# Kernel tuning notes

Hardware: AMD Instinct MI355X
Metric: run time of the kernel (lower is better)

The kernel has to match this reference:

```python
import jax, jax.numpy as jnp
import numpy as np

B, NMASK, DIM, HEADS = 8, 1024, 768, 12
HEAD_DIM = DIM // HEADS
SCALE = HEAD_DIM ** -0.5
NEG = -1e9  # finite stand-in for -inf to keep fully-masked rows NaN-free


def setup_inputs() -> dict:
    key = jax.random.key(0)
    ks = jax.random.split(key, 7)
    x = jax.random.normal(ks[0], (B, NMASK + 1, DIM), dtype=jnp.float32)
    # valid-prefix padding mask (realistic variable-length batch), lengths >= 1
    lengths = jax.random.randint(ks[1], (B,), 1, NMASK + 1)
    mask = jnp.arange(NMASK)[None, :] < lengths[:, None]  # (B, NMASK) bool
    w_qkv = jax.random.normal(ks[2], (DIM, 3 * DIM), dtype=jnp.float32) * (DIM ** -0.5)
    b_qkv = jax.random.normal(ks[3], (3 * DIM,), dtype=jnp.float32) * 0.02
    w_proj = jax.random.normal(ks[4], (DIM, DIM), dtype=jnp.float32) * (DIM ** -0.5)
    b_proj = jax.random.normal(ks[5], (DIM,), dtype=jnp.float32) * 0.02
    return {"x": x, "mask": mask, "w_qkv": w_qkv, "b_qkv": b_qkv,
            "w_proj": w_proj, "b_proj": b_proj}


def reference(x, mask, w_qkv, b_qkv, w_proj, b_proj):
    b, n, _ = x.shape
    qkv = x @ w_qkv + b_qkv                        # (b, n, 3*dim)
    qkv = qkv.reshape(b, n, 3, HEADS, HEAD_DIM)    # 'b n (qkv h d)'
    qkv = jnp.transpose(qkv, (2, 0, 3, 1, 4))      # (3, b, h, n, d)
    q, k, v = qkv[0], qkv[1], qkv[2]
    logits = jnp.einsum('bhid,bhjd->bhij', q, k) * SCALE
    m = jnp.pad(mask, ((0, 0), (1, 0)), constant_values=True)   # prepend CLS=True
    am = m[:, None, :] & m[:, :, None]             # (b, n, n)
    logits = jnp.where(am[:, None, :, :], logits, NEG)
    attn = jax.nn.softmax(logits, axis=-1)
    out = jnp.einsum('bhij,bhjd->bhid', attn, v)   # (b, h, n, d)
    out = jnp.transpose(out, (0, 2, 1, 3)).reshape(b, n, DIM)
    return out @ w_proj + b_proj                   # dropout is identity (eval/p=0)
```

## Files before the change

### kernel.cpp

```cpp
#include <hip/hip_runtime.h>
#include <stdint.h>

#define BATCH   8
#define NMASK_  1024
#define SEQ     1025
#define NPAD    1056
#define DIM     768
#define HEADS   12
#define HD      64
#define BHN     (BATCH*HEADS)
#define MROWS   (BATCH*SEQ)
#define K3      (3*DIM)

typedef unsigned short u16;
typedef __attribute__((ext_vector_type(8))) short s8v;
typedef __attribute__((ext_vector_type(4))) float f4v;
typedef __attribute__((ext_vector_type(4))) unsigned short u16x4;

__device__ __forceinline__ u16 rne_bf16(float f) {
  unsigned u = __float_as_uint(f);
  u += 0x7fffu + ((u >> 16) & 1u);
  return (u16)(u >> 16);
}
__device__ __forceinline__ float bf2f(u16 u) {
  return __uint_as_float(((unsigned)u) << 16);
}

__device__ __forceinline__ void gld16(const u16* g, u16* l) {
  __builtin_amdgcn_global_load_lds(
      (const __attribute__((address_space(1))) void*)g,
      (__attribute__((address_space(3))) void*)l, 16, 0, 0);
}

__device__ __forceinline__ void barrier_() {
  asm volatile("" ::: "memory");
  __builtin_amdgcn_s_barrier();
  asm volatile("" ::: "memory");
}

__global__ __launch_bounds__(256) void k_len(const int* __restrict__ mask,
                                             int* __restrict__ lens) {
  int b = blockIdx.x, t = threadIdx.x;
  int s = 0;
  for (int j = t; j < NMASK_; j += 256) s += (mask[b * NMASK_ + j] != 0) ? 1 : 0;
  __shared__ int red[256];
  red[t] = s; __syncthreads();
  for (int st = 128; st > 0; st >>= 1) { if (t < st) red[t] += red[t + st]; __syncthreads(); }
  if (t == 0) lens[b] = red[0] + 1;
}

__global__ __launch_bounds__(256) void k_cvt_x(const float* __restrict__ x,
                                               u16* __restrict__ xb, int n4) {
  int i = blockIdx.x * 256 + threadIdx.x;
  if (i >= n4) return;
  float4 v = ((const float4*)x)[i];
  u16x4 o;
  o[0] = rne_bf16(v.x); o[1] = rne_bf16(v.y); o[2] = rne_bf16(v.z); o[3] = rne_bf16(v.w);
  *(u16x4*)&xb[i * 4] = o;
}

__global__ __launch_bounds__(256) void k_wT(const float* __restrict__ w,
                                            u16* __restrict__ wT, int R, int C) {
  __shared__ float tile[32][33];
  int c0 = blockIdx.x * 32, r0 = blockIdx.y * 32;
  int tx = threadIdx.x & 31, ty = threadIdx.x >> 5;
  #pragma unroll
  for (int i = 0; i < 32; i += 8) tile[ty + i][tx] = w[(size_t)(r0 + ty + i) * C + c0 + tx];
  __syncthreads();
  #pragma unroll
  for (int i = 0; i < 32; i += 8)
    wT[(size_t)(c0 + ty + i) * R + r0 + tx] = rne_bf16(tile[tx][ty + i]);
}

__global__ __launch_bounds__(256) void k_zpad(u16* __restrict__ VT) {
  int idx = blockIdx.x * 256 + threadIdx.x;
  const int PADW = NPAD - SEQ;
  if (idx >= BHN * HD * PADW) return;
  int c = idx % PADW, rd = idx / PADW;
  VT[(size_t)rd * NPAD + SEQ + c] = 0;
}

__device__ __forceinline__ void gemm_ml128(const u16* __restrict__ A,
                                           const u16* __restrict__ Bt,
                                           int M, int m0, int n0,
                                           f4v acc[4][4], u16* smem) {
  const int t = threadIdx.x;
  const int w = t >> 6, l = t & 63, lg = l >> 4, lr = l & 15;
  const int wr = w >> 1, wc = w & 1;

  int rA0 = m0 + (t >> 2);       if (rA0 >= M) rA0 = M - 1;
  int rA1 = m0 + (t >> 2) + 64;  if (rA1 >= M) rA1 = M - 1;
  const u16* sA0 = A  + (size_t)rA0 * DIM + (t & 3) * 8;
  const u16* sA1 = A  + (size_t)rA1 * DIM + (t & 3) * 8;
  const u16* sB0 = Bt + (size_t)(n0 + (t >> 2)) * DIM + (t & 3) * 8;
  const u16* sB1 = Bt + (size_t)(n0 + (t >> 2) + 64) * DIM + (t & 3) * 8;
  const int dO0 = w * 512, dO1 = 2048 + w * 512;

  #pragma unroll
  for (int fm = 0; fm < 4; fm++)
    #pragma unroll
    for (int fn = 0; fn < 4; fn++) { f4v z = {0.f, 0.f, 0.f, 0.f}; acc[fm][fn] = z; }

  gld16(sA0, &smem[dO0]);        gld16(sA1, &smem[dO1]);
  gld16(sB0, &smem[8192 + dO0]); gld16(sB1, &smem[8192 + dO1]);

  const int NT = DIM / 32;
  for (int kt = 0; kt < NT; ++kt) {
    const int p = kt & 1;
    if (kt + 1 < NT) {
      const int ka = (kt + 1) * 32;
      const int nb = (p ^ 1) * 4096;
      gld16(sA0 + ka, &smem[nb + dO0]);        gld16(sA1 + ka, &smem[nb + dO1]);
      gld16(sB0 + ka, &smem[8192 + nb + dO0]); gld16(sB1 + ka, &smem[8192 + nb + dO1]);
      asm volatile("s_waitcnt vmcnt(4)" ::: "memory");
    } else {
      asm volatile("s_waitcnt vmcnt(0)" ::: "memory");
    }
    __builtin_amdgcn_sched_barrier(0);
    barrier_();
    const u16* lA = &smem[p * 4096];
    const u16* lB = &smem[8192 + p * 4096];
    s8v a[4], bb[4];
    #pragma unroll
    for (int fm = 0; fm < 4; fm++) a[fm] = *(const s8v*)&lA[(wr * 64 + fm * 16 + lr) * 32 + lg * 8];
    #pragma unroll
    for (int fn = 0; fn < 4; fn++) bb[fn] = *(const s8v*)&lB[(wc * 64 + fn * 16 + lr) * 32 + lg * 8];
    #pragma unroll
    for (int fm = 0; fm < 4; fm++)
      #pragma unroll
      for (int fn = 0; fn < 4; fn++)
        acc[fm][fn] = __builtin_amdgcn_mfma_f32_16x16x32_bf16(a[fm], bb[fn], acc[fm][fn], 0, 0, 0);
    barrier_();
  }
}

__global__ __launch_bounds__(256) void k_gemm_qkv(const u16* __restrict__ xb,
                                                  const u16* __restrict__ wqkvT,
                                                  const float* __restrict__ bqkv,
                                                  const int* __restrict__ lens,
                                                  u16* __restrict__ Q,
                                                  u16* __restrict__ Kb,
                                                  u16* __restrict__ VT) {
  __shared__ alignas(16) u16 smem[16384];
  int m0 = blockIdx.x * 128, n0 = blockIdx.y * 128;
  const int which = n0 / DIM;
  if (which < 2) {
    int b0 = m0 / SEQ, off = m0 - b0 * SEQ;
    bool spans = (m0 + 127) >= (b0 + 1) * SEQ;
    if (!spans && off >= lens[b0]) return;
  }
  f4v acc[4][4];
  gemm_ml128(xb, wqkvT, MROWS, m0, n0, acc, smem);
  const int t = threadIdx.x;
  const int w = t >> 6, l = t & 63, lg = l >> 4, lr = l & 15;
  const int wr = w >> 1, wc = w & 1;
  const int hbase = (n0 - which * DIM) >> 6;
  const float qs = (which == 0) ? 0.125f : 1.0f;

  __syncthreads();
  #pragma unroll
  for (int fn = 0; fn < 4; fn++) {
    int col = wc * 64 + fn * 16 + lr;
    float bias = bqkv[n0 + col];
    #pragma unroll
    for (int fm = 0; fm < 4; fm++)
      #pragma unroll
      for (int r = 0; r < 4; r++) {
        int row = wr * 64 + fm * 16 + lg * 4 + r;
        smem[row * 128 + col] = rne_bf16((acc[fm][fn][r] + bias) * qs);
      }
  }
  __syncthreads();

  if (which < 2) {
    u16* dst = (which == 0) ? Q : Kb;
    #pragma unroll
    for (int p = 0; p < 8; p++) {
      int c = p * 256 + t;
      int row = c >> 4, col = (c & 15) * 8;
      int gm = m0 + row;
      if (gm >= MROWS) continue;
      int b = gm / SEQ, n = gm - b * SEQ;
      int head = hbase + (col >> 6), d = col & 63;
      *(s8v*)&dst[((size_t)(b * HEADS + head) * NPAD + n) * HD + d] =
          *(const s8v*)&smem[row * 128 + col];
    }
  } else {
    #pragma unroll
    for (int p = 0; p < 8; p++) {
      int c = p * 256 + t;
      int d = c & 127, nb = c >> 7;
      int gm0 = m0 + nb * 8;
      if (gm0 >= MROWS) continue;
      int head = hbase + (d >> 6), dl = d & 63;
      int b0 = gm0 / SEQ;
      if (gm0 + 7 < MROWS && (gm0 + 7) < (b0 + 1) * SEQ) {
        s8v v;
        #pragma unroll
        for (int e = 0; e < 8; e++) v[e] = (short)smem[(nb * 8 + e) * 128 + d];
        int n = gm0 - b0 * SEQ;
        *(s8v*)&VT[((size_t)(b0 * HEADS + head) * HD + dl) * NPAD + n] = v;
      } else {
        for (int e = 0; e < 8; e++) {
          int gm = gm0 + e;
          if (gm >= MROWS) break;
          int b = gm / SEQ, n = gm - b * SEQ;
          VT[((size_t)(b * HEADS + head) * HD + dl) * NPAD + n] = smem[(nb * 8 + e) * 128 + d];
        }
      }
    }
  }
}

__global__ __launch_bounds__(256) void k_vmean(const u16* __restrict__ VT,
                                               float* __restrict__ vmean) {
  int bh = blockIdx.x, t = threadIdx.x;
  int d = t >> 2, part = t & 3;
  const u16* row = VT + (size_t)(bh * HD + d) * NPAD;
  float s = 0.f;
  for (int jc = part * 264; jc < part * 264 + 264; jc += 8) {
    if (jc + 8 <= SEQ) {
      s8v v = *(const s8v*)&row[jc];
      #pragma unroll
      for (int e = 0; e < 8; e++) s += bf2f((u16)v[e]);
    } else {
      for (int e = 0; e < 8; e++) if (jc + e < SEQ) s += bf2f(row[jc + e]);
    }
  }
  __shared__ float red[256];
  red[t] = s; __syncthreads();
  if (part == 0)
    vmean[bh * HD + d] = (red[t] + red[t + 1] + red[t + 2] + red[t + 3]) * (1.0f / (float)SEQ);
}

__global__ __launch_bounds__(256) void k_vproj(const float* __restrict__ vmean,
                                               const u16* __restrict__ wprojT,
                                               const float* __restrict__ bproj,
                                               float* __restrict__ vproj) {
  int gid = blockIdx.x * 4 + (threadIdx.x >> 6);
  if (gid >= BATCH * DIM) return;
  int b = gid / DIM, n = gid - b * DIM;
  int l = threadIdx.x & 63;
  const u16* wr = wprojT + (size_t)n * DIM;
  const float* vm = vmean + b * DIM;
  float s = 0.f;
  #pragma unroll
  for (int i = 0; i < DIM / 64; ++i)
    s += vm[l + i * 64] * bf2f(wr[l + i * 64]);
  #pragma unroll
  for (int off = 32; off >= 1; off >>= 1) s += __shfl_xor(s, off);
  if (l == 0) vproj[gid] = s + bproj[n];
}

__global__ __launch_bounds__(256) void k_attn(const u16* __restrict__ Q,
                                              const u16* __restrict__ Kb,
                                              const u16* __restrict__ VT,
                                              const int* __restrict__ lens,
                                              u16* __restrict__ aout) {
  int bh = blockIdx.x; int b = bh / HEADS, h = bh - b * HEADS;
  int Lp1 = lens[b];
  int q0 = blockIdx.y * 64;
  if (q0 >= Lp1) return;
  __shared__ alignas(16) u16 Kt[64 * 64];
  __shared__ alignas(16) u16 Vt[64 * 64];
  __shared__ alignas(16) u16 Pt[4][16 * 72];
  const int t = threadIdx.x, w = t >> 6, l = t & 63, lg = l >> 4, lr = l & 15;
  const u16* Qbh = Q  + (size_t)bh * NPAD * HD;
  const u16* Kbh = Kb + (size_t)bh * NPAD * HD;
  const u16* Vbh = VT + (size_t)bh * HD * NPAD;

  int qi = q0 + w * 16 + lr;
  s8v qf[2];
  qf[0] = *(const s8v*)&Qbh[(size_t)qi * HD +      lg * 8];
  qf[1] = *(const s8v*)&Qbh[(size_t)qi * HD + 32 + lg * 8];

  f4v o[4];
  #pragma unroll
  for (int fd = 0; fd < 4; fd++) { f4v z = {0.f, 0.f, 0.f, 0.f}; o[fd] = z; }
  float ssacc[4];
  #pragma unroll
  for (int r = 0; r < 4; r++) ssacc[r] = 0.f;

  const int js = t >> 2, cs = t & 3;
  const u16* kSrc = Kbh + (size_t)js * HD   + cs * 8;
  const u16* vSrc = Vbh + (size_t)js * NPAD + cs * 8;
  const int kDst0 = js * 64 + ((cs       ^ (js & 7)) * 8);
  const int kDst1 = js * 64 + (((cs + 4) ^ (js & 7)) * 8);
  s8v kr0, kr1, vr0, vr1;
  kr0 = *(const s8v*)(kSrc);        kr1 = *(const s8v*)(kSrc + 32);
  vr0 = *(const s8v*)(vSrc);        vr1 = *(const s8v*)(vSrc + 32);

  for (int j0 = 0; j0 < Lp1; j0 += 64) {
    __syncthreads();
    *(s8v*)&Kt[kDst0] = kr0;  *(s8v*)&Kt[kDst1] = kr1;
    *(s8v*)&Vt[kDst0] = vr0;  *(s8v*)&Vt[kDst1] = vr1;
    if (j0 + 64 < Lp1) {
      kr0 = *(const s8v*)(kSrc + (size_t)(j0 + 64) * HD);
      kr1 = *(const s8v*)(kSrc + (size_t)(j0 + 64) * HD + 32);
      vr0 = *(const s8v*)(vSrc + (j0 + 64));
      vr1 = *(const s8v*)(vSrc + (j0 + 64) + 32);
    }
    __syncthreads();

    f4v sf[4];
    #pragma unroll
    for (int jf = 0; jf < 4; jf++) { f4v z = {0.f,0.f,0.f,0.f}; sf[jf] = z; }
    __builtin_amdgcn_s_setprio(1);
    #pragma unroll
    for (int jf = 0; jf < 4; jf++) {
      int j = jf * 16 + lr;
      #pragma unroll
      for (int kf = 0; kf < 2; kf++) {
        s8v kfr = *(const s8v*)&Kt[j * 64 + (((kf * 4 + lg) ^ (j & 7)) * 8)];
        sf[jf] = __builtin_amdgcn_mfma_f32_16x16x32_bf16(qf[kf], kfr, sf[jf], 0, 0, 0);
      }
    }
    __builtin_amdgcn_s_setprio(0);

    u16* P = &Pt[w][0];
    if (j0 + 64 <= Lp1) {
      #pragma unroll
      for (int r = 0; r < 4; r++) {
        float e0 = __expf(sf[0][r]);
        float e1 = __expf(sf[1][r]);
        float e2 = __expf(sf[2][r]);
        float e3 = __expf(sf[3][r]);
        int prow = (lg * 4 + r) * 72;
        P[prow +      lr] = rne_bf16(e0);
        P[prow + 16 + lr] = rne_bf16(e1);
        P[prow + 32 + lr] = rne_bf16(e2);
        P[prow + 48 + lr] = rne_bf16(e3);
        ssacc[r] += (e0 + e1) + (e2 + e3);
      }
    } else {
      bool ok[4];
      #pragma unroll
      for (int jf = 0; jf < 4; jf++) ok[jf] = (j0 + jf * 16 + lr) < Lp1;
      #pragma unroll
      for (int r = 0; r < 4; r++) {
        float e0 = __expf(ok[0] ? sf[0][r] : -1e30f);
        float e1 = __expf(ok[1] ? sf[1][r] : -1e30f);
        float e2 = __expf(ok[2] ? sf[2][r] : -1e30f);
        float e3 = __expf(ok[3] ? sf[3][r] : -1e30f);
        int prow = (lg * 4 + r) * 72;
        P[prow +      lr] = rne_bf16(e0);
        P[prow + 16 + lr] = rne_bf16(e1);
        P[prow + 32 + lr] = rne_bf16(e2);
        P[prow + 48 + lr] = rne_bf16(e3);
        ssacc[r] += (e0 + e1) + (e2 + e3);
      }
    }
    asm volatile("s_waitcnt lgkmcnt(0)" ::: "memory");
    s8v pa[2];
    pa[0] = *(const s8v*)&P[lr * 72 +      lg * 8];
    pa[1] = *(const s8v*)&P[lr * 72 + 32 + lg * 8];
    __builtin_amdgcn_s_setprio(1);
    #pragma unroll
    for (int fd = 0; fd < 4; fd++) {
      int dv = fd * 16 + lr;
      #pragma unroll
      for (int kf = 0; kf < 2; kf++) {
        s8v vb = *(const s8v*)&Vt[dv * 64 + (((kf * 4 + lg) ^ (dv & 7)) * 8)];
        o[fd] = __builtin_amdgcn_mfma_f32_16x16x32_bf16(pa[kf], vb, o[fd], 0, 0, 0);
      }
    }
    __builtin_amdgcn_s_setprio(0);
  }

  float inv[4];
  #pragma unroll
  for (int r = 0; r < 4; r++) {
    float rs = ssacc[r];
    rs += __shfl_xor(rs, 1); rs += __shfl_xor(rs, 2);
    rs += __shfl_xor(rs, 4); rs += __shfl_xor(rs, 8);
    inv[r] = 1.0f / rs;
  }
  #pragma unroll
  for (int fd = 0; fd < 4; fd++)
    #pragma unroll
    for (int r = 0; r < 4; r++) {
      int i = q0 + w * 16 + lg * 4 + r;
      if (i < Lp1)
        aout[(size_t)(b * SEQ + i) * DIM + h * HD + fd * 16 + lr] = rne_bf16(o[fd][r] * inv[r]);
    }
}

__global__ __launch_bounds__(256) void k_bcast(const int* __restrict__ lens,
                                               const float* __restrict__ vproj,
                                               float* __restrict__ out) {
  int idx = blockIdx.x * 256 + threadIdx.x;
  if (idx >= MROWS * DIM / 4) return;
  int e4 = idx * 4;
  int b = e4 / (SEQ * DIM);
  int rem = e4 - b * (SEQ * DIM);
  int i = rem / DIM;
  if (i >= lens[b]) {
    int c = rem - i * DIM;
    const float* vp = &vproj[b * DIM + c];
    float4 v = { vp[0], vp[1], vp[2], vp[3] };
    ((float4*)out)[idx] = v;
  }
}

__global__ __launch_bounds__(256) void k_gemm_proj(const u16* __restrict__ aout,
                                                   const u16* __restrict__ wprojT,
                                                   const float* __restrict__ bproj,
                                                   const int* __restrict__ lens,
                                                   float* __restrict__ out) {
  __shared__ alignas(16) u16 smem[16384];
  int m0 = blockIdx.x * 128, n0 = blockIdx.y * 128;
  {
    int b0 = m0 / SEQ, off = m0 - b0 * SEQ;
    bool spans = (m0 + 127) >= (b0 + 1) * SEQ;
    if (!spans && off >= lens[b0]) return;
  }
  f4v acc[4][4];
  gemm_ml128(aout, wprojT, MROWS, m0, n0, acc, smem);
  const int t = threadIdx.x;
  const int w = t >> 6, l = t & 63, lg = l >> 4, lr = l & 15;
  const int wr = w >> 1, wc = w & 1;
  #pragma unroll
  for (int fn = 0; fn < 4; fn++) {
    int gc = n0 + wc * 64 + fn * 16 + lr;
    float bias = bproj[gc];
    #pragma unroll
    for (int fm = 0; fm < 4; fm++)
      #pragma unroll
      for (int r = 0; r < 4; r++) {
        int gm = m0 + wr * 64 + fm * 16 + lg * 4 + r;
        if (gm < MROWS) out[(size_t)gm * DIM + gc] = acc[fm][fn][r] + bias;
      }
  }
}

extern "C" void kernel_launch(void* const* d_in, const int* in_sizes, int n_in,
                              void* d_out, int out_size, void* d_ws, size_t ws_size,
                              hipStream_t stream) {
  const float* x      = (const float*)d_in[0];
  const int*   mask   = (const int*)  d_in[1];
  const float* w_qkv  = (const float*)d_in[2];
  const float* b_qkv  = (const float*)d_in[3];
  const float* w_proj = (const float*)d_in[4];
  const float* b_proj = (const float*)d_in[5];
  float* out = (float*)d_out;

  u16* xb     = (u16*)d_ws;
  u16* wqkvT  = xb    + (size_t)MROWS * DIM;
  u16* wprojT = wqkvT + (size_t)K3 * DIM;
  u16* Q      = wprojT + (size_t)DIM * DIM;
  u16* Kb     = Q     + (size_t)BHN * NPAD * HD;
  u16* VT     = Kb    + (size_t)BHN * NPAD * HD;
  float* vmean = (float*)(VT + (size_t)BHN * NPAD * HD);
  int* lens    = (int*)(vmean + BHN * HD);
  float* vproj = (float*)(lens + 256);
  u16* aout   = xb;

  k_len  <<<dim3(BATCH), dim3(256), 0, stream>>>(mask, lens);
  k_cvt_x<<<dim3((MROWS * DIM / 4 + 255) / 256), dim3(256), 0, stream>>>(x, xb, MROWS * DIM / 4);
  k_wT   <<<dim3(K3 / 32, DIM / 32), dim3(256), 0, stream>>>(w_qkv, wqkvT, DIM, K3);
  k_wT   <<<dim3(DIM / 32, DIM / 32), dim3(256), 0, stream>>>(w_proj, wprojT, DIM, DIM);
  k_zpad <<<dim3((BHN * HD * (NPAD - SEQ) + 255) / 256), dim3(256), 0, stream>>>(VT);
  k_gemm_qkv<<<dim3((MROWS + 127) / 128, K3 / 128), dim3(256), 0, stream>>>(xb, wqkvT, b_qkv, lens, Q, Kb, VT);
  k_vmean<<<dim3(BHN), dim3(256), 0, stream>>>(VT, vmean);
  k_vproj<<<dim3((BATCH * DIM + 3) / 4), dim3(256), 0, stream>>>(vmean, wprojT, b_proj, vproj);
  k_attn <<<dim3(BHN, (SEQ + 63) / 64), dim3(256), 0, stream>>>(Q, Kb, VT, lens, aout);
  k_gemm_proj<<<dim3((MROWS + 127) / 128, DIM / 128), dim3(256), 0, stream>>>(aout, wprojT, b_proj, lens, out);
  k_bcast<<<dim3((MROWS * DIM / 4 + 255) / 256), dim3(256), 0, stream>>>(lens, vproj, out);
}
```

Baseline: 159.5 us.

## Merge prep kernels, fuse masked-row broadcast into proj GEMM, use exp2

Combines the length reduction and V padding zeroing into one launch, merges the two weight transposes into one launch, and removes the separate broadcast pass by having the projection GEMM write vproj rows for masked tiles and masked rows itself. The Q scale now folds in log2(e) so the softmax can use exp2f instead of __expf. This cuts launch count and avoids a full extra pass over the output tensor. In exchange the GEMM epilogue does a per-element divide and lens lookup.

```diff
diff --git a/kernel.cpp b/kernel.cpp
--- a/kernel.cpp
+++ b/kernel.cpp
@@ -38,15 +38,24 @@
   asm volatile("" ::: "memory");
 }
 
-__global__ __launch_bounds__(256) void k_len(const int* __restrict__ mask,
-                                             int* __restrict__ lens) {
-  int b = blockIdx.x, t = threadIdx.x;
-  int s = 0;
-  for (int j = t; j < NMASK_; j += 256) s += (mask[b * NMASK_ + j] != 0) ? 1 : 0;
-  __shared__ int red[256];
-  red[t] = s; __syncthreads();
-  for (int st = 128; st > 0; st >>= 1) { if (t < st) red[t] += red[t + st]; __syncthreads(); }
-  if (t == 0) lens[b] = red[0] + 1;
+__global__ __launch_bounds__(256) void k_prep(const int* __restrict__ mask,
+                                              int* __restrict__ lens,
+                                              u16* __restrict__ VT) {
+  int bid = blockIdx.x, t = threadIdx.x;
+  if (bid < BATCH) {
+    int b = bid, s = 0;
+    for (int j = t; j < NMASK_; j += 256) s += (mask[b * NMASK_ + j] != 0) ? 1 : 0;
+    __shared__ int red[256];
+    red[t] = s; __syncthreads();
+    for (int st = 128; st > 0; st >>= 1) { if (t < st) red[t] += red[t + st]; __syncthreads(); }
+    if (t == 0) lens[b] = red[0] + 1;
+  } else {
+    int idx = (bid - BATCH) * 256 + t;
+    const int PADW = NPAD - SEQ;
+    if (idx >= BHN * HD * PADW) return;
+    int c = idx % PADW, rd = idx / PADW;
+    VT[(size_t)rd * NPAD + SEQ + c] = 0;
+  }
 }
 
 __global__ __launch_bounds__(256) void k_cvt_x(const float* __restrict__ x,
@@ -59,25 +68,23 @@
   *(u16x4*)&xb[i * 4] = o;
 }
 
-__global__ __launch_bounds__(256) void k_wT(const float* __restrict__ w,
-                                            u16* __restrict__ wT, int R, int C) {
+__global__ __launch_bounds__(256) void k_wT2(const float* __restrict__ wq,
+                                             const float* __restrict__ wp,
+                                             u16* __restrict__ wqT,
+                                             u16* __restrict__ wpT) {
   __shared__ float tile[32][33];
-  int c0 = blockIdx.x * 32, r0 = blockIdx.y * 32;
+  const bool isq = blockIdx.x < (K3 / 32);
+  const float* w = isq ? wq : wp;
+  u16* wT = isq ? wqT : wpT;
+  const int C = isq ? K3 : DIM;
+  int c0 = (isq ? blockIdx.x : blockIdx.x - K3 / 32) * 32, r0 = blockIdx.y * 32;
   int tx = threadIdx.x & 31, ty = threadIdx.x >> 5;
   #pragma unroll
   for (int i = 0; i < 32; i += 8) tile[ty + i][tx] = w[(size_t)(r0 + ty + i) * C + c0 + tx];
   __syncthreads();
   #pragma unroll
   for (int i = 0; i < 32; i += 8)
-    wT[(size_t)(c0 + ty + i) * R + r0 + tx] = rne_bf16(tile[tx][ty + i]);
-}
-
-__global__ __launch_bounds__(256) void k_zpad(u16* __restrict__ VT) {
-  int idx = blockIdx.x * 256 + threadIdx.x;
-  const int PADW = NPAD - SEQ;
-  if (idx >= BHN * HD * PADW) return;
-  int c = idx % PADW, rd = idx / PADW;
-  VT[(size_t)rd * NPAD + SEQ + c] = 0;
+    wT[(size_t)(c0 + ty + i) * DIM + r0 + tx] = rne_bf16(tile[tx][ty + i]);
 }
 
 __device__ __forceinline__ void gemm_ml128(const u16* __restrict__ A,
@@ -155,7 +162,7 @@
   const int w = t >> 6, l = t & 63, lg = l >> 4, lr = l & 15;
   const int wr = w >> 1, wc = w & 1;
   const int hbase = (n0 - which * DIM) >> 6;
-  const float qs = (which == 0) ? 0.125f : 1.0f;
+  const float qs = (which == 0) ? 0.18033688f : 1.0f;
 
   __syncthreads();
   #pragma unroll
@@ -321,10 +328,10 @@
     if (j0 + 64 <= Lp1) {
       #pragma unroll
       for (int r = 0; r < 4; r++) {
-        float e0 = __expf(sf[0][r]);
-        float e1 = __expf(sf[1][r]);
-        float e2 = __expf(sf[2][r]);
-        float e3 = __expf(sf[3][r]);
+        float e0 = exp2f(sf[0][r]);
+        float e1 = exp2f(sf[1][r]);
+        float e2 = exp2f(sf[2][r]);
+        float e3 = exp2f(sf[3][r]);
         int prow = (lg * 4 + r) * 72;
         P[prow +      lr] = rne_bf16(e0);
         P[prow + 16 + lr] = rne_bf16(e1);
@@ -338,10 +345,10 @@
       for (int jf = 0; jf < 4; jf++) ok[jf] = (j0 + jf * 16 + lr) < Lp1;
       #pragma unroll
       for (int r = 0; r < 4; r++) {
-        float e0 = __expf(ok[0] ? sf[0][r] : -1e30f);
-        float e1 = __expf(ok[1] ? sf[1][r] : -1e30f);
-        float e2 = __expf(ok[2] ? sf[2][r] : -1e30f);
-        float e3 = __expf(ok[3] ? sf[3][r] : -1e30f);
+        float e0 = exp2f(ok[0] ? sf[0][r] : -1e30f);
+        float e1 = exp2f(ok[1] ? sf[1][r] : -1e30f);
+        float e2 = exp2f(ok[2] ? sf[2][r] : -1e30f);
+        float e3 = exp2f(ok[3] ? sf[3][r] : -1e30f);
         int prow = (lg * 4 + r) * 72;
         P[prow +      lr] = rne_bf16(e0);
         P[prow + 16 + lr] = rne_bf16(e1);
@@ -385,34 +392,24 @@
     }
 }
 
-__global__ __launch_bounds__(256) void k_bcast(const int* __restrict__ lens,
-                                               const float* __restrict__ vproj,
-                                               float* __restrict__ out) {
-  int idx = blockIdx.x * 256 + threadIdx.x;
-  if (idx >= MROWS * DIM / 4) return;
-  int e4 = idx * 4;
-  int b = e4 / (SEQ * DIM);
-  int rem = e4 - b * (SEQ * DIM);
-  int i = rem / DIM;
-  if (i >= lens[b]) {
-    int c = rem - i * DIM;
-    const float* vp = &vproj[b * DIM + c];
-    float4 v = { vp[0], vp[1], vp[2], vp[3] };
-    ((float4*)out)[idx] = v;
-  }
-}
-
 __global__ __launch_bounds__(256) void k_gemm_proj(const u16* __restrict__ aout,
                                                    const u16* __restrict__ wprojT,
                                                    const float* __restrict__ bproj,
                                                    const int* __restrict__ lens,
+                                                   const float* __restrict__ vproj,
                                                    float* __restrict__ out) {
   __shared__ alignas(16) u16 smem[16384];
   int m0 = blockIdx.x * 128, n0 = blockIdx.y * 128;
-  {
-    int b0 = m0 / SEQ, off = m0 - b0 * SEQ;
-    bool spans = (m0 + 127) >= (b0 + 1) * SEQ;
-    if (!spans && off >= lens[b0]) return;
+  int b0 = m0 / SEQ, off = m0 - b0 * SEQ;
+  bool spans = (m0 + 127) >= (b0 + 1) * SEQ;
+  if (!spans && off >= lens[b0]) {
+    float4 v = ((const float4*)&vproj[b0 * DIM + n0])[threadIdx.x & 31];
+    for (int r = threadIdx.x >> 5; r < 128; r += 8) {
+      int gm = m0 + r;
+      if (gm < MROWS)
+        ((float4*)&out[(size_t)gm * DIM + n0])[threadIdx.x & 31] = v;
+    }
+    return;
   }
   f4v acc[4][4];
   gemm_ml128(aout, wprojT, MROWS, m0, n0, acc, smem);
@@ -428,7 +425,10 @@
       #pragma unroll
       for (int r = 0; r < 4; r++) {
         int gm = m0 + wr * 64 + fm * 16 + lg * 4 + r;
-        if (gm < MROWS) out[(size_t)gm * DIM + gc] = acc[fm][fn][r] + bias;
+        if (gm >= MROWS) continue;
+        int b = gm / SEQ, n = gm - b * SEQ;
+        float v = (n < lens[b]) ? (acc[fm][fn][r] + bias) : vproj[b * DIM + gc];
+        out[(size_t)gm * DIM + gc] = v;
       }
   }
 }
@@ -455,15 +455,13 @@
   float* vproj = (float*)(lens + 256);
   u16* aout   = xb;
 
-  k_len  <<<dim3(BATCH), dim3(256), 0, stream>>>(mask, lens);
+  const int ZBLK = (BHN * HD * (NPAD - SEQ) + 255) / 256;
+  k_prep <<<dim3(BATCH + ZBLK), dim3(256), 0, stream>>>(mask, lens, VT);
   k_cvt_x<<<dim3((MROWS * DIM / 4 + 255) / 256), dim3(256), 0, stream>>>(x, xb, MROWS * DIM / 4);
-  k_wT   <<<dim3(K3 / 32, DIM / 32), dim3(256), 0, stream>>>(w_qkv, wqkvT, DIM, K3);
-  k_wT   <<<dim3(DIM / 32, DIM / 32), dim3(256), 0, stream>>>(w_proj, wprojT, DIM, DIM);
-  k_zpad <<<dim3((BHN * HD * (NPAD - SEQ) + 255) / 256), dim3(256), 0, stream>>>(VT);
+  k_wT2  <<<dim3(K3 / 32 + DIM / 32, DIM / 32), dim3(256), 0, stream>>>(w_qkv, w_proj, wqkvT, wprojT);
   k_gemm_qkv<<<dim3((MROWS + 127) / 128, K3 / 128), dim3(256), 0, stream>>>(xb, wqkvT, b_qkv, lens, Q, Kb, VT);
   k_vmean<<<dim3(BHN), dim3(256), 0, stream>>>(VT, vmean);
   k_vproj<<<dim3((BATCH * DIM + 3) / 4), dim3(256), 0, stream>>>(vmean, wprojT, b_proj, vproj);
   k_attn <<<dim3(BHN, (SEQ + 63) / 64), dim3(256), 0, stream>>>(Q, Kb, VT, lens, aout);
-  k_gemm_proj<<<dim3((MROWS + 127) / 128, DIM / 128), dim3(256), 0, stream>>>(aout, wprojT, b_proj, lens, out);
-  k_bcast<<<dim3((MROWS * DIM / 4 + 255) / 256), dim3(256), 0, stream>>>(lens, vproj, out);
-}
+  k_gemm_proj<<<dim3((MROWS + 127) / 128, DIM / 128), dim3(256), 0, stream>>>(aout, wprojT, b_proj, lens, vproj, out);
+}
```

Result: slower. 166.4 us (+4.3%).
